# Optimization experiments

Hardware: AMD Instinct MI355X
Metric: run time of the kernel (lower is better)

Reference implementation:

```python
import jax, jax.numpy as jnp
import numpy as np
import math

N, H, V, K = 8192, 1024, 50257, 4096

def setup_inputs() -> dict:
    key = jax.random.key(0)
    k_in, k_tgt, k_noise, k_w, k_up = jax.random.split(key, 5)
    inp = jax.random.normal(k_in, (N, H), dtype=jnp.float32)
    target = jax.random.randint(k_tgt, (N,), 0, V)
    noise = jax.random.randint(k_noise, (K,), 0, V)  # alias-multinomial draw, fixed here
    stdv = 1.0 / math.sqrt(H)
    weight = jax.random.uniform(k_w, (V, H), dtype=jnp.float32, minval=-stdv, maxval=stdv)
    bias = jnp.full((V,), -math.log(V), dtype=jnp.float32)
    up = jax.random.uniform(k_up, (V,), dtype=jnp.float32, minval=1e-6, maxval=1.0)
    unigram_prob = up / jnp.sum(up)
    return {"input": inp, "weight": weight, "bias": bias,
            "unigram_prob": unigram_prob, "target": target, "noise": noise}

def reference(input, weight, bias, unigram_prob, target, noise):
    # 'train' mode of linear_nce
    w_target = weight[target]                      # [N, H] gather
    b_target = bias[target]                        # [N]
    pmt = jnp.exp(jnp.sum(input * w_target, axis=1) + b_target)   # [N]
    pnt = unigram_prob[target]                     # [N]
    w_noise = weight[noise]                        # [K, H] gather
    b_noise = bias[noise]                          # [K]
    pmn = jnp.exp(jnp.einsum('nh,kh->nk', input, w_noise) + b_noise)  # [N, K]
    pnn = jnp.broadcast_to(unigram_prob[noise][None, :], (input.shape[0], noise.shape[0]))  # [N, K]
    return (pmt, pnt, pmn, pnn)
```

## Files before the change

### kernel.cpp

```cpp
#include <hip/hip_runtime.h>
#include <hip/hip_bf16.h>

#define NROWS 8192
#define HDIM  1024
#define VDIM  50257
#define KNOISE 4096

typedef short  bf16x8 __attribute__((ext_vector_type(8)));
typedef float  f32x4  __attribute__((ext_vector_type(4)));

__device__ __forceinline__ unsigned short f2bf(float x) {
    union { float f; unsigned int u; } v; v.f = x;
    unsigned int r = (v.u + 0x7fffu + ((v.u >> 16) & 1u)) >> 16;
    return (unsigned short)r;
}

__device__ __forceinline__ void gload16(const void* g, void* l) {
    __builtin_amdgcn_global_load_lds(
        (const __attribute__((address_space(1))) void*)g,
        (__attribute__((address_space(3))) void*)l, 16, 0, 0);
}

__global__ __launch_bounds__(256) void prep_kernel(
        const float* __restrict__ input,
        const float* __restrict__ weight,
        const float* __restrict__ bias,
        const float* __restrict__ unigram,
        const int* __restrict__ target,
        const int* __restrict__ noise,
        unsigned short* __restrict__ in_bf,
        unsigned short* __restrict__ wn_bf,
        float* __restrict__ bn,
        float* __restrict__ un,
        float* __restrict__ out_pmt,
        float* __restrict__ out_pnt) {
    const int tid = threadIdx.x;
    if (blockIdx.x < NROWS) {
        const int row = blockIdx.x;
        const int t = target[row];
        float4 a = ((const float4*)(input + (size_t)row * HDIM))[tid];
        ushort4 o;
        o.x = f2bf(a.x); o.y = f2bf(a.y); o.z = f2bf(a.z); o.w = f2bf(a.w);
        ((ushort4*)(in_bf + (size_t)row * HDIM))[tid] = o;
        float4 w = ((const float4*)(weight + (size_t)t * HDIM))[tid];
        float s = a.x * w.x + a.y * w.y + a.z * w.z + a.w * w.w;
        #pragma unroll
        for (int off = 32; off > 0; off >>= 1) s += __shfl_down(s, off);
        __shared__ float red[4];
        if ((tid & 63) == 0) red[tid >> 6] = s;
        __syncthreads();
        if (tid == 0) {
            float tot = red[0] + red[1] + red[2] + red[3];
            out_pmt[row] = expf(tot + bias[t]);
            out_pnt[row] = unigram[t];
        }
    } else {
        const int r = blockIdx.x - NROWS;
        const int idx = noise[r];
        float4 v = ((const float4*)(weight + (size_t)idx * HDIM))[tid];
        ushort4 o;
        o.x = f2bf(v.x); o.y = f2bf(v.y); o.z = f2bf(v.z); o.w = f2bf(v.w);
        ((ushort4*)(wn_bf + (size_t)r * HDIM))[tid] = o;
        if (tid == 0) { bn[r] = bias[idx]; un[r] = unigram[idx]; }
    }
}

#define BM 256
#define BN 256
#define ASLOT 16384
#define BRING_OFF 81920
#define EPS_LD 68
#define SMEM_DYN 163840

__global__ __launch_bounds__(512, 2) void gemm_nce_kernel(
        const unsigned short* __restrict__ A,
        const unsigned short* __restrict__ Bt,
        const float* __restrict__ bn,
        const float* __restrict__ un,
        float* __restrict__ pmn,
        float* __restrict__ pnn) {
    extern __shared__ char smem[];

    const int tid  = threadIdx.x;
    const int wave = tid >> 6;
    const int lane = tid & 63;
    const int wm   = wave >> 2;
    const int wn2  = wave & 3;
    const int r    = lane & 15;
    const int q    = lane >> 4;
    const int swz  = (r & 7) << 4;

    const int bid  = blockIdx.x;
    const int swzb = (bid & 7) * 64 + (bid >> 3);
    const int row0 = (swzb & 31) * BM;
    const int col0 = (swzb >> 5) * BN;

    const int lrow   = tid >> 3;
    const int lchunk = tid & 7;
    const int lsc    = lchunk ^ (lrow & 7);
    const unsigned short* gA = A  + (size_t)(row0 + lrow) * HDIM + lsc * 8;
    const unsigned short* gB = Bt + (size_t)(col0 + lrow) * HDIM + lsc * 8;
    char* ldsAw = smem + wave * 1024;
    char* ldsBw = smem + BRING_OFF + wave * 1024;

    auto stageA = [&](int h) {
        const unsigned short* g = gA + (size_t)((h & 1) * 128) * HDIM + (h >> 1) * 64;
        char* l = ldsAw + (h % 5) * ASLOT;
        gload16(g, l);
        gload16(g + 64 * HDIM, l + 8192);
    };
    auto stageB = [&](int h) {
        const unsigned short* g = gB + (size_t)((h & 1) * 128) * HDIM + (h >> 1) * 64;
        char* l = ldsBw + (h % 5) * ASLOT;
        gload16(g, l);
        gload16(g + 64 * HDIM, l + 8192);
    };

    const int rrd = q;
    const int crd = r * 4;
    const float4 unv4 = *(const float4*)&un[col0 + wn2 * 64 + crd];
    float bnv[4];
    #pragma unroll
    for (int ni = 0; ni < 4; ni++)
        bnv[ni] = bn[col0 + wn2 * 64 + ni * 16 + r];
    float* pnn_base = pnn + (size_t)(row0 + wm * 128 + rrd) * KNOISE
                          + col0 + wn2 * 64 + crd;

    f32x4 acc[8][4];
    #pragma unroll
    for (int mi = 0; mi < 8; mi++)
        #pragma unroll
        for (int ni = 0; ni < 4; ni++)
            acc[mi][ni] = (f32x4){0.f, 0.f, 0.f, 0.f};

    stageA(0); stageB(0); stageA(1); stageB(1); stageA(2); stageB(2);
    asm volatile("s_waitcnt vmcnt(4)" ::: "memory");
    __builtin_amdgcn_s_barrier();

    int slotA = wm;
    int slotB = wn2 >> 1;
    const int koff0 = (q * 16) ^ swz;
    const int koff1 = (64 + q * 16) ^ swz;

    for (int t = 0; t < 16; ++t) {
        const char* As = smem + slotA * ASLOT;
        const char* Bs = smem + BRING_OFF + slotB * ASLOT;
        #pragma unroll
        for (int p = 0; p < 4; ++p) {
            const int mih = p >> 1, nih = p & 1;
            bf16x8 af[4][2], bv[2][2];
            #pragma unroll
            for (int m4 = 0; m4 < 4; ++m4) {
                const int rb = (mih * 64 + m4 * 16 + r) << 7;
                af[m4][0] = *(const bf16x8*)(As + rb + koff0);
                af[m4][1] = *(const bf16x8*)(As + rb + koff1);
            }
            #pragma unroll
            for (int n2 = 0; n2 < 2; ++n2) {
                const int cb = ((wn2 & 1) * 64 + nih * 32 + n2 * 16 + r) << 7;
                bv[n2][0] = *(const bf16x8*)(Bs + cb + koff0);
                bv[n2][1] = *(const bf16x8*)(Bs + cb + koff1);
            }
            if (p == 0)      { if (t <= 14) stageA(2 * t + 3); }
            else if (p == 1) { if (t <= 14) stageB(2 * t + 3); }
            else if (p == 2) {
                float* pb = pnn_base + (size_t)(8 * t) * KNOISE;
                *(float4*)pb = unv4;
                *(float4*)(pb + 4 * KNOISE) = unv4;
                if (t <= 13) stageA(2 * t + 4);
            } else           { if (t <= 13) stageB(2 * t + 4); }

            __builtin_amdgcn_s_barrier();
            asm volatile("s_waitcnt lgkmcnt(0)" ::: "memory");
            __builtin_amdgcn_sched_barrier(0);
            __builtin_amdgcn_s_setprio(1);
            #pragma unroll
            for (int m4 = 0; m4 < 4; ++m4)
                #pragma unroll
                for (int n2 = 0; n2 < 2; ++n2) {
                    f32x4 c = acc[mih * 4 + m4][nih * 2 + n2];
                    c = __builtin_amdgcn_mfma_f32_16x16x32_bf16(af[m4][0], bv[n2][0], c, 0, 0, 0);
                    c = __builtin_amdgcn_mfma_f32_16x16x32_bf16(af[m4][1], bv[n2][1], c, 0, 0, 0);
                    acc[mih * 4 + m4][nih * 2 + n2] = c;
                }
            __builtin_amdgcn_s_setprio(0);
            __builtin_amdgcn_sched_barrier(0);
            if (p == 3) {
                if (t < 14)       { asm volatile("s_waitcnt vmcnt(6)" ::: "memory"); }
                else if (t == 14) { asm volatile("s_waitcnt vmcnt(2)" ::: "memory"); }
            }
            __builtin_amdgcn_s_barrier();
        }
        slotA += 2; if (slotA >= 5) slotA -= 5;
        slotB += 2; if (slotB >= 5) slotB -= 5;
    }

    float* eps = (float*)smem + wave * (16 * EPS_LD);
    #pragma unroll
    for (int mi = 0; mi < 8; ++mi) {
        #pragma unroll
        for (int ni = 0; ni < 4; ++ni)
            #pragma unroll
            for (int j = 0; j < 4; ++j)
                eps[(q * 4 + j) * EPS_LD + ni * 16 + r] = __expf(acc[mi][ni][j] + bnv[ni]);
        __builtin_amdgcn_s_waitcnt(0xc07f);
        #pragma unroll
        for (int j = 0; j < 4; ++j) {
            float4 v = *(float4*)&eps[(rrd * 4 + j) * EPS_LD + crd];
            size_t off = (size_t)(row0 + wm * 128 + mi * 16 + rrd * 4 + j) * KNOISE
                       + col0 + wn2 * 64 + crd;
            *(float4*)&pmn[off] = v;
        }
        __builtin_amdgcn_s_waitcnt(0xc07f);
    }
}

extern "C" void kernel_launch(void* const* d_in, const int* in_sizes, int n_in,
                              void* d_out, int out_size, void* d_ws, size_t ws_size,
                              hipStream_t stream) {
    const float* input   = (const float*)d_in[0];
    const float* weight  = (const float*)d_in[1];
    const float* bias    = (const float*)d_in[2];
    const float* unigram = (const float*)d_in[3];
    const int*   target  = (const int*)d_in[4];
    const int*   noise   = (const int*)d_in[5];

    unsigned short* in_bf = (unsigned short*)d_ws;
    unsigned short* wn_bf = in_bf + (size_t)NROWS * HDIM;
    float* bn = (float*)(wn_bf + (size_t)KNOISE * HDIM);
    float* un = bn + KNOISE;

    float* out = (float*)d_out;
    float* o_pmt = out;
    float* o_pnt = out + NROWS;
    float* o_pmn = out + 2 * NROWS;
    float* o_pnn = o_pmn + (size_t)NROWS * KNOISE;

    static bool attr_done = false;
    if (!attr_done) {
        (void)hipFuncSetAttribute(reinterpret_cast<const void*>(gemm_nce_kernel),
                                  hipFuncAttributeMaxDynamicSharedMemorySize,
                                  SMEM_DYN);
        attr_done = true;
    }

    prep_kernel<<<NROWS + KNOISE, 256, 0, stream>>>(
        input, weight, bias, unigram, target, noise,
        in_bf, wn_bf, bn, un, o_pmt, o_pnt);

    gemm_nce_kernel<<<512, 512, SMEM_DYN, stream>>>(
        in_bf, wn_bf, bn, un, o_pmn, o_pnn);
}
```

Measured before the change: 447.6 us.

## Reorder MFMA quadrants to reuse LDS fragments and use nontemporal output stores

Each K-step's four MFMA phases now run in a snake order (A-top×B-left, A-top×B-right, A-bottom×B-right, A-bottom×B-left), so A and B fragments loaded from LDS are reused across consecutive phases. This drops some LDS reads, and the last phase skips the LDS wait entirely. The large pmn and pnn output writes become nontemporal stores to reduce cache pollution, and the bias loads move after the main loop to shorten live ranges. Keeping extra B fragments in registers raises register pressure, which could reduce occupancy.

```diff
diff --git a/kernel.cpp b/kernel.cpp
--- a/kernel.cpp
+++ b/kernel.cpp
@@ -118,82 +118,141 @@
 
     const int rrd = q;
     const int crd = r * 4;
-    const float4 unv4 = *(const float4*)&un[col0 + wn2 * 64 + crd];
+    const f32x4 unv4 = *(const f32x4*)&un[col0 + wn2 * 64 + crd];
+    float* pnn_base = pnn + (size_t)(row0 + wm * 128 + rrd) * KNOISE
+                          + col0 + wn2 * 64 + crd;
+
+    f32x4 acc[8][4];
+    #pragma unroll
+    for (int mi = 0; mi < 8; mi++)
+        #pragma unroll
+        for (int ni = 0; ni < 4; ni++)
+            acc[mi][ni] = (f32x4){0.f, 0.f, 0.f, 0.f};
+
+    stageA(0); stageB(0); stageA(1); stageB(1); stageA(2); stageB(2);
+    asm volatile("s_waitcnt vmcnt(4)" ::: "memory");
+    __builtin_amdgcn_s_barrier();
+
+    int slotA = wm;
+    int slotB = wn2 >> 1;
+    const int koff0 = (q * 16) ^ swz;
+    const int koff1 = (64 + q * 16) ^ swz;
+
+    for (int t = 0; t < 16; ++t) {
+        const char* As = smem + slotA * ASLOT;
+        const char* Bs = smem + BRING_OFF + slotB * ASLOT;
+
+        bf16x8 af[4][2], bv[2][2][2];
+
+        #pragma unroll
+        for (int m4 = 0; m4 < 4; ++m4) {
+            const int rb = (m4 * 16 + r) << 7;
+            af[m4][0] = *(const bf16x8*)(As + rb + koff0);
+            af[m4][1] = *(const bf16x8*)(As + rb + koff1);
+        }
+        #pragma unroll
+        for (int n2 = 0; n2 < 2; ++n2) {
+            const int cb = ((wn2 & 1) * 64 + n2 * 16 + r) << 7;
+            bv[0][n2][0] = *(const bf16x8*)(Bs + cb + koff0);
+            bv[0][n2][1] = *(const bf16x8*)(Bs + cb + koff1);
+        }
+        if (t <= 14) stageA(2 * t + 3);
+        __builtin_amdgcn_s_barrier();
+        asm volatile("s_waitcnt lgkmcnt(0)" ::: "memory");
+        __builtin_amdgcn_sched_barrier(0);
+        __builtin_amdgcn_s_setprio(1);
+        #pragma unroll
+        for (int m4 = 0; m4 < 4; ++m4)
+            #pragma unroll
+            for (int n2 = 0; n2 < 2; ++n2) {
+                f32x4 c = acc[m4][n2];
+                c = __builtin_amdgcn_mfma_f32_16x16x32_bf16(af[m4][0], bv[0][n2][0], c, 0, 0, 0);
+                c = __builtin_amdgcn_mfma_f32_16x16x32_bf16(af[m4][1], bv[0][n2][1], c, 0, 0, 0);
+                acc[m4][n2] = c;
+            }
+        __builtin_amdgcn_s_setprio(0);
+        __builtin_amdgcn_sched_barrier(0);
+        __builtin_amdgcn_s_barrier();
+
+        #pragma unroll
+        for (int n2 = 0; n2 < 2; ++n2) {
+            const int cb = ((wn2 & 1) * 64 + 32 + n2 * 16 + r) << 7;
+            bv[1][n2][0] = *(const bf16x8*)(Bs + cb + koff0);
+            bv[1][n2][1] = *(const bf16x8*)(Bs + cb + koff1);
+        }
+        if (t <= 14) stageB(2 * t + 3);
+        __builtin_amdgcn_s_barrier();
+        asm volatile("s_waitcnt lgkmcnt(0)" ::: "memory");
+        __builtin_amdgcn_sched_barrier(0);
+        __builtin_amdgcn_s_setprio(1);
+        #pragma unroll
+        for (int m4 = 0; m4 < 4; ++m4)
+            #pragma unroll
+            for (int n2 = 0; n2 < 2; ++n2) {
+                f32x4 c = acc[m4][2 + n2];
+                c = __builtin_amdgcn_mfma_f32_16x16x32_bf16(af[m4][0], bv[1][n2][0], c, 0, 0, 0);
+                c = __builtin_amdgcn_mfma_f32_16x16x32_bf16(af[m4][1], bv[1][n2][1], c, 0, 0, 0);
+                acc[m4][2 + n2] = c;
+            }
+        __builtin_amdgcn_s_setprio(0);
+        __builtin_amdgcn_sched_barrier(0);
+        __builtin_amdgcn_s_barrier();
+
+        #pragma unroll
+        for (int m4 = 0; m4 < 4; ++m4) {
+            const int rb = (64 + m4 * 16 + r) << 7;
+            af[m4][0] = *(const bf16x8*)(As + rb + koff0);
+            af[m4][1] = *(const bf16x8*)(As + rb + koff1);
+        }
+        {
+            float* pb = pnn_base + (size_t)(8 * t) * KNOISE;
+            __builtin_nontemporal_store(unv4, (f32x4*)pb);
+            __builtin_nontemporal_store(unv4, (f32x4*)(pb + 4 * KNOISE));
+        }
+        if (t <= 13) stageA(2 * t + 4);
+        __builtin_amdgcn_s_barrier();
+        asm volatile("s_waitcnt lgkmcnt(0)" ::: "memory");
+        __builtin_amdgcn_sched_barrier(0);
+        __builtin_amdgcn_s_setprio(1);
+        #pragma unroll
+        for (int m4 = 0; m4 < 4; ++m4)
+            #pragma unroll
+            for (int n2 = 0; n2 < 2; ++n2) {
+                f32x4 c = acc[4 + m4][2 + n2];
+                c = __builtin_amdgcn_mfma_f32_16x16x32_bf16(af[m4][0], bv[1][n2][0], c, 0, 0, 0);
+                c = __builtin_amdgcn_mfma_f32_16x16x32_bf16(af[m4][1], bv[1][n2][1], c, 0, 0, 0);
+                acc[4 + m4][2 + n2] = c;
+            }
+        __builtin_amdgcn_s_setprio(0);
+        __builtin_amdgcn_sched_barrier(0);
+        __builtin_amdgcn_s_barrier();
+
+        if (t <= 13) stageB(2 * t + 4);
+        __builtin_amdgcn_s_barrier();
+        __builtin_amdgcn_s_setprio(1);
+        #pragma unroll
+        for (int m4 = 0; m4 < 4; ++m4)
+            #pragma unroll
+            for (int n2 = 0; n2 < 2; ++n2) {
+                f32x4 c = acc[4 + m4][n2];
+                c = __builtin_amdgcn_mfma_f32_16x16x32_bf16(af[m4][0], bv[0][n2][0], c, 0, 0, 0);
+                c = __builtin_amdgcn_mfma_f32_16x16x32_bf16(af[m4][1], bv[0][n2][1], c, 0, 0, 0);
+                acc[4 + m4][n2] = c;
+            }
+        __builtin_amdgcn_s_setprio(0);
+        __builtin_amdgcn_sched_barrier(0);
+        if (t < 14)       { asm volatile("s_waitcnt vmcnt(6)" ::: "memory"); }
+        else if (t == 14) { asm volatile("s_waitcnt vmcnt(2)" ::: "memory"); }
+        __builtin_amdgcn_s_barrier();
+
+        slotA += 2; if (slotA >= 5) slotA -= 5;
+        slotB += 2; if (slotB >= 5) slotB -= 5;
+    }
+
     float bnv[4];
     #pragma unroll
     for (int ni = 0; ni < 4; ni++)
         bnv[ni] = bn[col0 + wn2 * 64 + ni * 16 + r];
-    float* pnn_base = pnn + (size_t)(row0 + wm * 128 + rrd) * KNOISE
-                          + col0 + wn2 * 64 + crd;
-
-    f32x4 acc[8][4];
-    #pragma unroll
-    for (int mi = 0; mi < 8; mi++)
-        #pragma unroll
-        for (int ni = 0; ni < 4; ni++)
-            acc[mi][ni] = (f32x4){0.f, 0.f, 0.f, 0.f};
-
-    stageA(0); stageB(0); stageA(1); stageB(1); stageA(2); stageB(2);
-    asm volatile("s_waitcnt vmcnt(4)" ::: "memory");
-    __builtin_amdgcn_s_barrier();
-
-    int slotA = wm;
-    int slotB = wn2 >> 1;
-    const int koff0 = (q * 16) ^ swz;
-    const int koff1 = (64 + q * 16) ^ swz;
-
-    for (int t = 0; t < 16; ++t) {
-        const char* As = smem + slotA * ASLOT;
-        const char* Bs = smem + BRING_OFF + slotB * ASLOT;
-        #pragma unroll
-        for (int p = 0; p < 4; ++p) {
-            const int mih = p >> 1, nih = p & 1;
-            bf16x8 af[4][2], bv[2][2];
-            #pragma unroll
-            for (int m4 = 0; m4 < 4; ++m4) {
-                const int rb = (mih * 64 + m4 * 16 + r) << 7;
-                af[m4][0] = *(const bf16x8*)(As + rb + koff0);
-                af[m4][1] = *(const bf16x8*)(As + rb + koff1);
-            }
-            #pragma unroll
-            for (int n2 = 0; n2 < 2; ++n2) {
-                const int cb = ((wn2 & 1) * 64 + nih * 32 + n2 * 16 + r) << 7;
-                bv[n2][0] = *(const bf16x8*)(Bs + cb + koff0);
-                bv[n2][1] = *(const bf16x8*)(Bs + cb + koff1);
-            }
-            if (p == 0)      { if (t <= 14) stageA(2 * t + 3); }
-            else if (p == 1) { if (t <= 14) stageB(2 * t + 3); }
-            else if (p == 2) {
-                float* pb = pnn_base + (size_t)(8 * t) * KNOISE;
-                *(float4*)pb = unv4;
-                *(float4*)(pb + 4 * KNOISE) = unv4;
-                if (t <= 13) stageA(2 * t + 4);
-            } else           { if (t <= 13) stageB(2 * t + 4); }
-
-            __builtin_amdgcn_s_barrier();
-            asm volatile("s_waitcnt lgkmcnt(0)" ::: "memory");
-            __builtin_amdgcn_sched_barrier(0);
-            __builtin_amdgcn_s_setprio(1);
-            #pragma unroll
-            for (int m4 = 0; m4 < 4; ++m4)
-                #pragma unroll
-                for (int n2 = 0; n2 < 2; ++n2) {
-                    f32x4 c = acc[mih * 4 + m4][nih * 2 + n2];
-                    c = __builtin_amdgcn_mfma_f32_16x16x32_bf16(af[m4][0], bv[n2][0], c, 0, 0, 0);
-                    c = __builtin_amdgcn_mfma_f32_16x16x32_bf16(af[m4][1], bv[n2][1], c, 0, 0, 0);
-                    acc[mih * 4 + m4][nih * 2 + n2] = c;
-                }
-            __builtin_amdgcn_s_setprio(0);
-            __builtin_amdgcn_sched_barrier(0);
-            if (p == 3) {
-                if (t < 14)       { asm volatile("s_waitcnt vmcnt(6)" ::: "memory"); }
-                else if (t == 14) { asm volatile("s_waitcnt vmcnt(2)" ::: "memory"); }
-            }
-            __builtin_amdgcn_s_barrier();
-        }
-        slotA += 2; if (slotA >= 5) slotA -= 5;
-        slotB += 2; if (slotB >= 5) slotB -= 5;
-    }
 
     float* eps = (float*)smem + wave * (16 * EPS_LD);
     #pragma unroll
@@ -206,10 +265,10 @@
         __builtin_amdgcn_s_waitcnt(0xc07f);
         #pragma unroll
         for (int j = 0; j < 4; ++j) {
-            float4 v = *(float4*)&eps[(rrd * 4 + j) * EPS_LD + crd];
+            f32x4 v = *(f32x4*)&eps[(rrd * 4 + j) * EPS_LD + crd];
             size_t off = (size_t)(row0 + wm * 128 + mi * 16 + rrd * 4 + j) * KNOISE
                        + col0 + wn2 * 64 + crd;
-            *(float4*)&pmn[off] = v;
+            __builtin_nontemporal_store(v, (f32x4*)&pmn[off]);
         }
         __builtin_amdgcn_s_waitcnt(0xc07f);
     }
```

After: 439.2 us. Within noise of the previous version (-1.9%).
